# Performance work log

Measured on AMD Instinct MI355X. Metric: run time of the kernel, lower is better.

Reference implementation:

```python
import jax, jax.numpy as jnp
import numpy as np

N_NODES = 100000
N_EDGES = 1600000
N_GRAPHS = 4096
IN_FEATS = 64
HIDDEN = 128


def setup_inputs() -> dict:
    key = jax.random.key(0)
    ks = jax.random.split(key, 16)
    feats_node = jax.random.normal(ks[0], (N_NODES, IN_FEATS), dtype=jnp.float32)
    feats_graph = jax.random.normal(ks[1], (N_GRAPHS, 3), dtype=jnp.float32)
    src = jax.random.randint(ks[2], (N_EDGES,), 0, N_NODES, dtype=jnp.int32)
    dst = jax.random.randint(ks[3], (N_EDGES,), 0, N_NODES, dtype=jnp.int32)
    node2graph = jnp.sort(jax.random.randint(ks[4], (N_NODES,), 0, N_GRAPHS, dtype=jnp.int32))
    # weights stored as [in, out] (torch Linear W.T); init per module: std=0.5 weights, bias ~ N(0.01, 0.001)
    def w(k, shape):
        return jax.random.normal(k, shape, dtype=jnp.float32) * 0.5
    def b(k, shape):
        return 0.01 + 0.001 * jax.random.normal(k, shape, dtype=jnp.float32)
    return {
        'feats_node': feats_node, 'feats_graph': feats_graph,
        'src': src, 'dst': dst, 'node2graph': node2graph,
        'W1': w(ks[5], (IN_FEATS, HIDDEN)), 'b1': b(ks[6], (HIDDEN,)),
        'W2': w(ks[7], (HIDDEN, HIDDEN)), 'b2': b(ks[8], (HIDDEN,)),
        'W3': w(ks[9], (HIDDEN, HIDDEN)), 'b3': b(ks[10], (HIDDEN,)),
        'L1w': w(ks[11], (HIDDEN + 3, 2 * HIDDEN)), 'L1b': b(ks[12], (2 * HIDDEN,)),
        'L2w': w(ks[13], (2 * HIDDEN, HIDDEN)), 'L2b': b(ks[14], (HIDDEN,)),
        'L3w': w(ks[15], (HIDDEN, 1)), 'L3b': b(jax.random.fold_in(key, 99), (1,)),
    }


def _graph_conv(x, W, b, src, dst, norm_out, norm_in):
    # DGL GraphConv(norm='both'): h_i = (sum_{j->i} x_j * d_out(j)^-1/2) * d_in(i)^-1/2 @ W + b
    m = (x * norm_out)[src]                       # [E, F] gather
    agg = jax.ops.segment_sum(m, dst, num_segments=N_NODES)
    return (agg * norm_in) @ W + b


def reference(feats_node, feats_graph, W1, b1, W2, b2, W3, b3, L1w, L1b, L2w, L2b, L3w, L3b, src, dst, node2graph):
    ones = jnp.ones((N_EDGES,), dtype=jnp.float32)
    deg_out = jax.ops.segment_sum(ones, src, num_segments=N_NODES)
    deg_in = jax.ops.segment_sum(ones, dst, num_segments=N_NODES)
    norm_out = jnp.clip(deg_out, 1.0, None)[:, None] ** -0.5  # [N,1]
    norm_in = jnp.clip(deg_in, 1.0, None)[:, None] ** -0.5

    x = jax.nn.selu(_graph_conv(feats_node, W1, b1, src, dst, norm_out, norm_in))
    x = jax.nn.selu(_graph_conv(x, W2, b2, src, dst, norm_out, norm_in))
    y_node = _graph_conv(x, W3, b3, src, dst, norm_out, norm_in)

    y_sum = jax.ops.segment_sum(y_node, node2graph, num_segments=N_GRAPHS)  # readout 'sum'
    y = jnp.concatenate([y_sum, feats_graph], axis=1)  # [G, H+3]
    y = jax.nn.selu(y @ L1w + L1b)
    y = jax.nn.selu(y @ L2w + L2b)
    return (y @ L3w + L3b).reshape(-1)
```

## Files before the change

kernel.cpp:

```cpp
#include <hip/hip_runtime.h>
#include <math.h>

#define SELU_ALPHA 1.6732632423543772f
#define SELU_SCALE 1.0507009873554805f

#define NBLK 512
#define MAXBKT 512

typedef __attribute__((ext_vector_type(8))) short bf16x8;
typedef __attribute__((ext_vector_type(4))) float f32x4;

__device__ __forceinline__ float selu_f(float x) {
    return SELU_SCALE * (x > 0.f ? x : SELU_ALPHA * expm1f(x));
}

__device__ __forceinline__ float bf2f(unsigned short u) {
    return __uint_as_float(((unsigned)u) << 16);
}
__device__ __forceinline__ unsigned short f2bf(float f) {
    unsigned u = __float_as_uint(f);
    unsigned r = (u + 0x7fffu + ((u >> 16) & 1u)) >> 16;
    return (unsigned short)r;
}

#define SCAN_B 1024

__global__ __launch_bounds__(256) void scan_block_sums(const int* __restrict__ in,
                                                       int* __restrict__ bsums, int n) {
    __shared__ int s[256];
    int b = blockIdx.x, t = threadIdx.x;
    int base = b * SCAN_B;
    int sum = 0;
    for (int i = t; i < SCAN_B; i += 256) {
        int idx = base + i;
        sum += (idx < n) ? in[idx] : 0;
    }
    s[t] = sum; __syncthreads();
    for (int off = 128; off > 0; off >>= 1) {
        if (t < off) s[t] += s[t + off];
        __syncthreads();
    }
    if (t == 0) bsums[b] = s[0];
}

__global__ __launch_bounds__(256) void scan_apply2(const int* __restrict__ in,
                                                   const int* __restrict__ bsums,
                                                   int* __restrict__ out, int n, int nb) {
    __shared__ int sb[512];
    __shared__ int s[256];
    __shared__ int blockoff;
    int b = blockIdx.x, t = threadIdx.x;

    int orig0 = (t < nb) ? bsums[t] : 0;
    int orig1 = (t + 256 < nb) ? bsums[t + 256] : 0;
    sb[t] = orig0; sb[t + 256] = orig1;
    __syncthreads();
    for (int off = 1; off < 512; off <<= 1) {
        int v0 = (t >= off) ? sb[t - off] : 0;
        int v1 = (t + 256 >= off) ? sb[t + 256 - off] : 0;
        __syncthreads();
        sb[t] += v0; sb[t + 256] += v1;
        __syncthreads();
    }
    if (t == (b & 255)) {
        bool hi = b >= 256;
        int incl = hi ? sb[t + 256] : sb[t];
        int orig = hi ? orig1 : orig0;
        blockoff = incl - orig;
    }
    __syncthreads();

    int idx0 = b * SCAN_B + t * 4;
    int v[4]; int tsum = 0;
    #pragma unroll
    for (int k = 0; k < 4; ++k) {
        int idx = idx0 + k;
        v[k] = (idx < n) ? in[idx] : 0;
        tsum += v[k];
    }
    s[t] = tsum; __syncthreads();
    for (int off = 1; off < 256; off <<= 1) {
        int x = (t >= off) ? s[t - off] : 0;
        __syncthreads();
        s[t] += x;
        __syncthreads();
    }
    int run = s[t] - tsum + blockoff;
    #pragma unroll
    for (int k = 0; k < 4; ++k) {
        int idx = idx0 + k;
        if (idx < n) out[idx] = run;
        run += v[k];
    }
}

__global__ __launch_bounds__(256) void hist_prep_kernel(
        const int* __restrict__ src, const int* __restrict__ dst,
        int* __restrict__ cntD, int* __restrict__ cntS, int E, int nbkt,
        const float* __restrict__ W1, const float* __restrict__ W2,
        const float* __restrict__ W3, const float* __restrict__ b3,
        const float* __restrict__ L1w, const float* __restrict__ L2w,
        unsigned short* __restrict__ Wt1, unsigned short* __restrict__ Wt2,
        unsigned short* __restrict__ W1c, unsigned short* __restrict__ L2w16) {
    if (blockIdx.x >= NBLK) {
        const int s0 = 128 * 64;
        const int s1 = 128 * 128;
        const int s2 = 128 * 256;
        const int s3 = 3 * 256;
        const int s4 = 256;
        const int s5 = 256 * 128 / 4;
        int i = (blockIdx.x - NBLK) * 256 + threadIdx.x;
        if (i < s0) { int col = i / 64, k = i % 64; Wt1[i] = f2bf(W1[k * 128 + col]); return; }
        i -= s0;
        if (i < s1) { int col = i / 128, k = i % 128; Wt2[i] = f2bf(W2[k * 128 + col]); return; }
        i -= s1;
        if (i < s2) {
            int k = i >> 8, o = i & 255;
            float acc = 0.f;
            #pragma unroll 8
            for (int m = 0; m < 128; ++m)
                acc += W3[k * 128 + m] * L1w[m * 256 + o];
            W1c[k * 256 + o] = f2bf(acc);
            return;
        }
        i -= s2;
        if (i < s3) {
            int r = i >> 8, o = i & 255;
            W1c[(128 + r) * 256 + o] = f2bf(L1w[(128 + r) * 256 + o]);
            return;
        }
        i -= s3;
        if (i < s4) {
            int o = i;
            float acc = 0.f;
            #pragma unroll 8
            for (int m = 0; m < 128; ++m)
                acc += b3[m] * L1w[m * 256 + o];
            W1c[131 * 256 + o] = f2bf(acc);
            return;
        }
        i -= s4;
        if (i < s5) {
            float4 v = reinterpret_cast<const float4*>(L2w)[i];
            unsigned short o[4] = { f2bf(v.x), f2bf(v.y), f2bf(v.z), f2bf(v.w) };
            reinterpret_cast<uint2*>(L2w16)[i] = *reinterpret_cast<uint2*>(o);
        }
        return;
    }
    __shared__ int hD[MAXBKT];
    __shared__ int hS[MAXBKT];
    int bb = blockIdx.x, t = threadIdx.x;
    for (int k = t; k < MAXBKT; k += 256) { hD[k] = 0; hS[k] = 0; }
    __syncthreads();
    int chunk = E / NBLK;
    int beg = bb * chunk, end = beg + chunk;
    for (int i = beg + t; i < end; i += 256) {
        atomicAdd(&hD[((unsigned)dst[i]) >> 8], 1);
        atomicAdd(&hS[((unsigned)src[i]) >> 8], 1);
    }
    __syncthreads();
    for (int k = t; k < nbkt; k += 256) {
        cntD[k * NBLK + bb] = hD[k];
        cntS[k * NBLK + bb] = hS[k];
    }
}

__global__ __launch_bounds__(256) void scatter_kernel(
        const int* __restrict__ src, const int* __restrict__ dst,
        const int* __restrict__ cntD, const int* __restrict__ cntS,
        unsigned* __restrict__ pairs, int* __restrict__ sbufm, int E, int nbkt) {
    __shared__ int cD[MAXBKT];
    __shared__ int cS[MAXBKT];
    int bb = blockIdx.x, t = threadIdx.x;
    for (int k = t; k < nbkt; k += 256) {
        cD[k] = cntD[k * NBLK + bb];
        cS[k] = cntS[k * NBLK + bb];
    }
    __syncthreads();
    int chunk = E / NBLK;
    int beg = bb * chunk, end = beg + chunk;
    for (int i = beg + t; i < end; i += 256) {
        unsigned s = (unsigned)src[i], d = (unsigned)dst[i];
        int pD = atomicAdd(&cD[d >> 8], 1);
        pairs[pD] = s | ((d & 255u) << 24);
        int pS = atomicAdd(&cS[s >> 8], 1);
        sbufm[pS] = (int)s;
    }
}

__global__ __launch_bounds__(256) void bucket_build_kernel(
        const int* __restrict__ sbufm, const unsigned* __restrict__ pairs,
        const int* __restrict__ cntD, const int* __restrict__ cntS,
        const float* __restrict__ feats,
        float* __restrict__ norm_out, unsigned short* __restrict__ feats16,
        int* __restrict__ row_start, int* __restrict__ deg_in,
        int* __restrict__ csr_src, int N, int E, int nbkt) {
    __shared__ int hist[256];
    __shared__ int sc[256];
    __shared__ int cur[256];
    __shared__ float nrm[256];
    int b = blockIdx.x, t = threadIdx.x;
    int node = (b << 8) + t;
    int node0 = b << 8;

    {
        int base = cntS[b * NBLK];
        int end = (b + 1 < nbkt) ? cntS[(b + 1) * NBLK] : 2 * E;
        hist[t] = 0; __syncthreads();
        for (int i = base + t; i < end; i += 256)
            atomicAdd(&hist[sbufm[i] & 255], 1);
        __syncthreads();
        float no = 1.f / sqrtf(fmaxf((float)hist[t], 1.f));
        nrm[t] = no;
        if (node < N) norm_out[node] = no;
        __syncthreads();
    }

    {
        int cnt = min(256, N - node0);
        for (int i = t; i < cnt * 8; i += 256) {
            int nl = i >> 3, c = i & 7;
            float no = nrm[nl];
            const float* fp = feats + (size_t)(node0 + nl) * 64 + c * 8;
            float4 a = *reinterpret_cast<const float4*>(fp);
            float4 bv = *reinterpret_cast<const float4*>(fp + 4);
            unsigned short o[8] = { f2bf(a.x * no), f2bf(a.y * no), f2bf(a.z * no), f2bf(a.w * no),
                                    f2bf(bv.x * no), f2bf(bv.y * no), f2bf(bv.z * no), f2bf(bv.w * no) };
            *reinterpret_cast<float4*>(feats16 + (size_t)(node0 + nl) * 64 + c * 8) =
                *reinterpret_cast<float4*>(o);
        }
        __syncthreads();
    }

    {
        int base = cntD[b * NBLK];
        int end = (b + 1 < nbkt) ? cntD[(b + 1) * NBLK] : E;
        hist[t] = 0; __syncthreads();
        for (int i = base + t; i < end; i += 256)
            atomicAdd(&hist[(pairs[i] >> 24) & 255], 1);
        __syncthreads();
        int v = hist[t];
        sc[t] = v; __syncthreads();
        for (int off = 1; off < 256; off <<= 1) {
            int x = (t >= off) ? sc[t - off] : 0;
            __syncthreads();
            sc[t] += x;
            __syncthreads();
        }
        int ex = sc[t] - v;
        cur[t] = base + ex;
        if (node < N) { row_start[node] = base + ex; deg_in[node] = v; }
        __syncthreads();
        for (int i = base + t; i < end; i += 256) {
            unsigned p = pairs[i];
            int pos = atomicAdd(&cur[(p >> 24) & 255], 1);
            csr_src[pos] = (int)(p & 0xFFFFFFu);
        }
    }
}

template<int TPG, int FIN>
__global__ __launch_bounds__(256) void csr_agg_kernel(
        const unsigned short* __restrict__ x, const int* __restrict__ row_start,
        const int* __restrict__ deg_in, const int* __restrict__ csr_src,
        unsigned short* __restrict__ agg, int N) {
    const int GPB = 256 / TPG;
    int g = threadIdx.x / TPG;
    int j = threadIdx.x % TPG;
    int n = blockIdx.x * GPB + g;
    if (n >= N) return;
    const int lane = threadIdx.x & 63;
    const int gbase = lane & ~(TPG - 1);
    int beg = row_start[n];
    int dg = deg_in[n];
    int end = beg + dg;
    float nin = 1.f / sqrtf(fmaxf((float)dg, 1.f));
    float acc[8] = {0.f, 0.f, 0.f, 0.f, 0.f, 0.f, 0.f, 0.f};
    int myIdx = (beg + j < end) ? csr_src[beg + j] : 0;
    for (int c = beg; c < end; c += TPG) {
        int cnt = end - c;
        int nxtIdx = (c + TPG + j < end) ? csr_src[c + TPG + j] : 0;
        float4 v[TPG];
        #pragma unroll
        for (int t = 0; t < TPG; ++t) {
            if (t < cnt) {
                int s = __shfl(myIdx, gbase + t, 64);
                v[t] = *reinterpret_cast<const float4*>(&x[(size_t)s * FIN + j * 8]);
            }
        }
        #pragma unroll
        for (int t = 0; t < TPG; ++t) {
            if (t < cnt) {
                const unsigned short* u = reinterpret_cast<const unsigned short*>(&v[t]);
                #pragma unroll
                for (int k = 0; k < 8; ++k) acc[k] += bf2f(u[k]);
            }
        }
        myIdx = nxtIdx;
    }
    unsigned short ov[8];
    #pragma unroll
    for (int k = 0; k < 8; ++k) ov[k] = f2bf(acc[k] * nin);
    *reinterpret_cast<float4*>(&agg[(size_t)n * FIN + j * 8]) = *reinterpret_cast<float4*>(ov);
}

template<int FIN, bool SELU, bool SCALE_OUT>
__global__ __launch_bounds__(256, 4) void gemm_mfma_kernel(
        const unsigned short* __restrict__ agg16,
        const unsigned short* __restrict__ Wt,
        const float* __restrict__ b,
        const float* __restrict__ norm_out,
        unsigned short* __restrict__ out,
        int N) {
    const int PAD = 8;
    const int LDW = FIN + PAD;
    const int CH = FIN / 8;
    __shared__ unsigned short sW[128 * LDW];
    const int tid = threadIdx.x;
    const int wave = tid >> 6, lane = tid & 63;
    const int wr = (wave >> 1) * 64;
    const int wc = (wave & 1) * 64;
    const int n0 = blockIdx.x * 128;

    for (int i = tid; i < 128 * CH; i += 256) {
        int col = i / CH, kc = i % CH;
        *reinterpret_cast<float4*>(&sW[col * LDW + kc * 8]) =
            *reinterpret_cast<const float4*>(&Wt[col * FIN + kc * 8]);
    }
    __syncthreads();

    const int l16 = lane & 15;
    const int lk = (lane >> 4) * 8;
    const bf16x8 zero8 = (bf16x8){0,0,0,0,0,0,0,0};
    f32x4 acc[4][4];
    #pragma unroll
    for (int mi = 0; mi < 4; ++mi)
        #pragma unroll
        for (int ci = 0; ci < 4; ++ci)
            acc[mi][ci] = (f32x4){0.f, 0.f, 0.f, 0.f};

    #pragma unroll
    for (int k0 = 0; k0 < FIN; k0 += 32) {
        bf16x8 a[4], w[4];
        #pragma unroll
        for (int mi = 0; mi < 4; ++mi) {
            int n = n0 + wr + mi * 16 + l16;
            a[mi] = (n < N)
                ? *reinterpret_cast<const bf16x8*>(&agg16[(size_t)n * FIN + k0 + lk])
                : zero8;
        }
        #pragma unroll
        for (int ci = 0; ci < 4; ++ci)
            w[ci] = *reinterpret_cast<const bf16x8*>(&sW[(wc + ci * 16 + l16) * LDW + k0 + lk]);
        #pragma unroll
        for (int mi = 0; mi < 4; ++mi)
            #pragma unroll
            for (int ci = 0; ci < 4; ++ci)
                acc[mi][ci] = __builtin_amdgcn_mfma_f32_16x16x32_bf16(
                    a[mi], w[ci], acc[mi][ci], 0, 0, 0);
    }

    const int rbase = (lane >> 4) * 4;
    #pragma unroll
    for (int ci = 0; ci < 4; ++ci) {
        int col = wc + ci * 16 + l16;
        float bias = b[col];
        #pragma unroll
        for (int mi = 0; mi < 4; ++mi) {
            #pragma unroll
            for (int r = 0; r < 4; ++r) {
                int n = n0 + wr + mi * 16 + rbase + r;
                if (n < N) {
                    float v = acc[mi][ci][r] + bias;
                    if (SELU) v = selu_f(v);
                    if (SCALE_OUT) v *= norm_out[n];
                    out[(size_t)n * 128 + col] = f2bf(v);
                }
            }
        }
    }
}

__global__ __launch_bounds__(128) void readout_kernel(
        const unsigned short* __restrict__ y, const int* __restrict__ n2g,
        float* __restrict__ gsum, float* __restrict__ cntf, int N, int G) {
    int g = blockIdx.x;
    int o = threadIdx.x;
    if (g >= G) return;
    int beg, end;
    {
        int lo = 0, hi = N;
        while (lo < hi) { int m = (lo + hi) >> 1; if (n2g[m] < g) lo = m + 1; else hi = m; }
        beg = lo;
        lo = beg; hi = N;
        while (lo < hi) { int m = (lo + hi) >> 1; if (n2g[m] < g + 1) lo = m + 1; else hi = m; }
        end = lo;
    }
    float acc = 0.f;
    for (int n = beg; n < end; ++n)
        acc += bf2f(y[(size_t)n * 128 + o]);
    gsum[(size_t)g * 128 + o] = acc;
    if (o == 0) cntf[g] = (float)(end - beg);
}

__global__ __launch_bounds__(256) void mlp_head_kernel(
        const float* __restrict__ gsum, const float* __restrict__ fg,
        const float* __restrict__ cntf,
        const unsigned short* __restrict__ W1c,
        const float* __restrict__ L1b,
        const unsigned short* __restrict__ L2w16,
        const float* __restrict__ L2b,
        const float* __restrict__ L3w, const float* __restrict__ L3b,
        float* __restrict__ out, int G) {
    __shared__ unsigned short sW[132 * 256];
    __shared__ float sIn[16][132];
    __shared__ float sY1[16][256];
    __shared__ float sL3[128];
    __shared__ float red[16][2];
    int tid = threadIdx.x;
    int g0 = blockIdx.x * 16;

    for (int i = tid; i < 132 * 256 / 2; i += 256)
        reinterpret_cast<unsigned*>(sW)[i] = reinterpret_cast<const unsigned*>(W1c)[i];
    for (int i = tid; i < 16 * 132; i += 256) {
        int g = i / 132, k = i - g * 132;
        float v = 0.f;
        if (g0 + g < G) {
            if (k < 128)       v = gsum[(size_t)(g0 + g) * 128 + k];
            else if (k < 131)  v = fg[(size_t)(g0 + g) * 3 + (k - 128)];
            else               v = cntf[g0 + g];
        }
        sIn[g][k] = v;
    }
    __syncthreads();
    {
        float bias = L1b[tid];
        for (int g = 0; g < 16; ++g) {
            float acc = bias;
            #pragma unroll 4
            for (int k = 0; k < 132; ++k)
                acc += sIn[g][k] * bf2f(sW[k * 256 + tid]);
            sY1[g][tid] = selu_f(acc);
        }
    }
    __syncthreads();

    for (int i = tid; i < 256 * 128 / 2; i += 256)
        reinterpret_cast<unsigned*>(sW)[i] = reinterpret_cast<const unsigned*>(L2w16)[i];
    if (tid < 128) sL3[tid] = L3w[tid];
    __syncthreads();
    {
        int o = tid & 127;
        int half = tid >> 7;
        int lane = tid & 63;
        int wv = tid >> 6;
        float bias = L2b[o];
        float w3 = sL3[o];
        for (int gg = 0; gg < 8; ++gg) {
            int g = half * 8 + gg;
            float acc = bias;
            #pragma unroll 8
            for (int k = 0; k < 256; ++k)
                acc += sY1[g][k] * bf2f(sW[k * 128 + o]);
            float v = selu_f(acc) * w3;
            #pragma unroll
            for (int off = 32; off > 0; off >>= 1)
                v += __shfl_down(v, off, 64);
            if (lane == 0) red[g][wv & 1] = v;
        }
    }
    __syncthreads();
    if (tid < 16) {
        int g = g0 + tid;
        if (g < G) out[g] = red[tid][0] + red[tid][1] + L3b[0];
    }
}

extern "C" void kernel_launch(void* const* d_in, const int* in_sizes, int n_in,
                              void* d_out, int out_size, void* d_ws, size_t ws_size,
                              hipStream_t stream) {
    const float* feats_node  = (const float*)d_in[0];
    const float* feats_graph = (const float*)d_in[1];
    const int*   src         = (const int*)d_in[2];
    const int*   dst         = (const int*)d_in[3];
    const int*   node2graph  = (const int*)d_in[4];
    const float* W1 = (const float*)d_in[5];
    const float* b1 = (const float*)d_in[6];
    const float* W2 = (const float*)d_in[7];
    const float* b2 = (const float*)d_in[8];
    const float* W3 = (const float*)d_in[9];
    const float* b3 = (const float*)d_in[10];
    const float* L1w = (const float*)d_in[11];
    const float* L1b = (const float*)d_in[12];
    const float* L2w = (const float*)d_in[13];
    const float* L2b = (const float*)d_in[14];
    const float* L3w = (const float*)d_in[15];
    const float* L3b = (const float*)d_in[16];

    const int N = in_sizes[0] / 64;
    const int G = in_sizes[1] / 3;
    const int E = in_sizes[2];
    const int NBKT = (N + 255) >> 8;
    const int nmat = NBKT * NBLK;
    const int nscan = 2 * nmat;
    const int NBsc = (nscan + SCAN_B - 1) / SCAN_B;

    int* iws = (int*)d_ws;
    int* deg_in_i  = iws;
    int* row_start = deg_in_i + N;
    int* bsums     = row_start + N;
    int* cntD      = bsums + 512;
    int* cntS      = cntD + nmat;
    int* csr_src   = cntS + nmat;

    float* norm_out = (float*)(csr_src + E);

    unsigned short* feats16 = (unsigned short*)(norm_out + N);
    unsigned short* x16     = feats16 + (size_t)N * 64;
    unsigned short* agg16   = x16 + (size_t)N * 128;
    unsigned short* Wt1     = agg16 + (size_t)N * 128;
    unsigned short* Wt2     = Wt1 + 128 * 64;
    unsigned short* W1c     = Wt2 + 128 * 128;
    unsigned short* L2w16   = W1c + 132 * 256;

    float* gsum = (float*)(L2w16 + 256 * 128);
    float* cntf = gsum + (size_t)G * 128;

    unsigned* pairs = (unsigned*)(((uintptr_t)agg16 + 15) & ~(uintptr_t)15);
    int*      sbuf  = (int*)(pairs + E);
    int*      sbufm = sbuf - E;

    float* out = (float*)d_out;

    {
        const int wtotal = 128 * 64 + 128 * 128 + 128 * 256 + 3 * 256 + 256 + 256 * 128 / 4;
        const int wblocks = (wtotal + 255) / 256;
        hist_prep_kernel<<<NBLK + wblocks, 256, 0, stream>>>(
            src, dst, cntD, cntS, E, NBKT,
            W1, W2, W3, b3, L1w, L2w, Wt1, Wt2, W1c, L2w16);
    }

    scan_block_sums<<<NBsc, 256, 0, stream>>>(cntD, bsums, nscan);
    scan_apply2<<<NBsc, 256, 0, stream>>>(cntD, bsums, cntD, nscan, NBsc);
    scatter_kernel<<<NBLK, 256, 0, stream>>>(src, dst, cntD, cntS, pairs, sbufm, E, NBKT);

    bucket_build_kernel<<<NBKT, 256, 0, stream>>>(
        sbufm, pairs, cntD, cntS, feats_node,
        norm_out, feats16, row_start, deg_in_i, csr_src, N, E, NBKT);

    const int gemm_grid = (N + 127) / 128;

    csr_agg_kernel<8, 64><<<(N + 31) / 32, 256, 0, stream>>>(
        feats16, row_start, deg_in_i, csr_src, agg16, N);
    gemm_mfma_kernel<64, true, true><<<gemm_grid, 256, 0, stream>>>(
        agg16, Wt1, b1, norm_out, x16, N);

    csr_agg_kernel<16, 128><<<(N + 15) / 16, 256, 0, stream>>>(
        x16, row_start, deg_in_i, csr_src, agg16, N);
    gemm_mfma_kernel<128, true, true><<<gemm_grid, 256, 0, stream>>>(
        agg16, Wt2, b2, norm_out, x16, N);

    csr_agg_kernel<16, 128><<<(N + 15) / 16, 256, 0, stream>>>(
        x16, row_start, deg_in_i, csr_src, agg16, N);

    readout_kernel<<<G, 128, 0, stream>>>(agg16, node2graph, gsum, cntf, N, G);

    mlp_head_kernel<<<(G + 15) / 16, 256, 0, stream>>>(
        gsum, feats_graph, cntf, W1c, L1b, L2w16, L2b, L3w, L3b, out, G);
}
```

Before: 382.0 us.

## Fuse graph readout and MLP head into one per-graph kernel

Merges the readout kernel and the batched MLP head into one kernel with one block per graph. Each block sums its node rows with two halves, then runs the L1 and L2 layers reading weights straight from global memory/L2 instead of staging them in LDS. This removes a launch and the gsum/cntf round trip through global memory. In exchange, every graph block re-reads the full weight matrices (about 130 KB) through cache, where before one staged copy served 16 graphs.

```diff
diff --git a/kernel.cpp b/kernel.cpp
--- a/kernel.cpp
+++ b/kernel.cpp
@@ -381,12 +381,24 @@
     }
 }
 
-__global__ __launch_bounds__(128) void readout_kernel(
-        const unsigned short* __restrict__ y, const int* __restrict__ n2g,
-        float* __restrict__ gsum, float* __restrict__ cntf, int N, int G) {
+__global__ __launch_bounds__(256) void head_kernel(
+        const unsigned short* __restrict__ agg16,
+        const int* __restrict__ n2g,
+        const float* __restrict__ fg,
+        const unsigned short* __restrict__ W1c,
+        const float* __restrict__ L1b,
+        const unsigned short* __restrict__ L2w16,
+        const float* __restrict__ L2b,
+        const float* __restrict__ L3w, const float* __restrict__ L3b,
+        float* __restrict__ out, int N, int G) {
+    __shared__ float sIn[132];
+    __shared__ float sY1[256];
+    __shared__ float sPair[256];
+    __shared__ float sRed[2];
     int g = blockIdx.x;
-    int o = threadIdx.x;
     if (g >= G) return;
+    int tid = threadIdx.x;
+
     int beg, end;
     {
         int lo = 0, hi = N;
@@ -396,84 +408,47 @@
         while (lo < hi) { int m = (lo + hi) >> 1; if (n2g[m] < g + 1) lo = m + 1; else hi = m; }
         end = lo;
     }
-    float acc = 0.f;
-    for (int n = beg; n < end; ++n)
-        acc += bf2f(y[(size_t)n * 128 + o]);
-    gsum[(size_t)g * 128 + o] = acc;
-    if (o == 0) cntf[g] = (float)(end - beg);
-}
-
-__global__ __launch_bounds__(256) void mlp_head_kernel(
-        const float* __restrict__ gsum, const float* __restrict__ fg,
-        const float* __restrict__ cntf,
-        const unsigned short* __restrict__ W1c,
-        const float* __restrict__ L1b,
-        const unsigned short* __restrict__ L2w16,
-        const float* __restrict__ L2b,
-        const float* __restrict__ L3w, const float* __restrict__ L3b,
-        float* __restrict__ out, int G) {
-    __shared__ unsigned short sW[132 * 256];
-    __shared__ float sIn[16][132];
-    __shared__ float sY1[16][256];
-    __shared__ float sL3[128];
-    __shared__ float red[16][2];
-    int tid = threadIdx.x;
-    int g0 = blockIdx.x * 16;
-
-    for (int i = tid; i < 132 * 256 / 2; i += 256)
-        reinterpret_cast<unsigned*>(sW)[i] = reinterpret_cast<const unsigned*>(W1c)[i];
-    for (int i = tid; i < 16 * 132; i += 256) {
-        int g = i / 132, k = i - g * 132;
-        float v = 0.f;
-        if (g0 + g < G) {
-            if (k < 128)       v = gsum[(size_t)(g0 + g) * 128 + k];
-            else if (k < 131)  v = fg[(size_t)(g0 + g) * 3 + (k - 128)];
-            else               v = cntf[g0 + g];
-        }
-        sIn[g][k] = v;
-    }
-    __syncthreads();
-    {
-        float bias = L1b[tid];
-        for (int g = 0; g < 16; ++g) {
-            float acc = bias;
-            #pragma unroll 4
-            for (int k = 0; k < 132; ++k)
-                acc += sIn[g][k] * bf2f(sW[k * 256 + tid]);
-            sY1[g][tid] = selu_f(acc);
-        }
-    }
-    __syncthreads();
-
-    for (int i = tid; i < 256 * 128 / 2; i += 256)
-        reinterpret_cast<unsigned*>(sW)[i] = reinterpret_cast<const unsigned*>(L2w16)[i];
-    if (tid < 128) sL3[tid] = L3w[tid];
-    __syncthreads();
-    {
-        int o = tid & 127;
-        int half = tid >> 7;
-        int lane = tid & 63;
-        int wv = tid >> 6;
-        float bias = L2b[o];
-        float w3 = sL3[o];
-        for (int gg = 0; gg < 8; ++gg) {
-            int g = half * 8 + gg;
-            float acc = bias;
-            #pragma unroll 8
-            for (int k = 0; k < 256; ++k)
-                acc += sY1[g][k] * bf2f(sW[k * 128 + o]);
-            float v = selu_f(acc) * w3;
-            #pragma unroll
-            for (int off = 32; off > 0; off >>= 1)
-                v += __shfl_down(v, off, 64);
-            if (lane == 0) red[g][wv & 1] = v;
-        }
-    }
-    __syncthreads();
-    if (tid < 16) {
-        int g = g0 + tid;
-        if (g < G) out[g] = red[tid][0] + red[tid][1] + L3b[0];
-    }
+    {
+        int col = tid & 127, h = tid >> 7;
+        float acc = 0.f;
+        for (int n = beg + h; n < end; n += 2)
+            acc += bf2f(agg16[(size_t)n * 128 + col]);
+        sPair[tid] = acc;
+    }
+    __syncthreads();
+    if (tid < 128) sIn[tid] = sPair[tid] + sPair[tid + 128];
+    else if (tid < 131) sIn[tid] = fg[(size_t)g * 3 + (tid - 128)];
+    else if (tid == 131) sIn[131] = (float)(end - beg);
+    __syncthreads();
+
+    {
+        float acc = L1b[tid];
+        #pragma unroll 4
+        for (int k = 0; k < 132; ++k)
+            acc += sIn[k] * bf2f(W1c[k * 256 + tid]);
+        sY1[tid] = selu_f(acc);
+    }
+    __syncthreads();
+
+    {
+        int o = tid & 127, h = tid >> 7;
+        float acc = 0.f;
+        int k0 = h * 128;
+        #pragma unroll 8
+        for (int k = 0; k < 128; ++k)
+            acc += sY1[k0 + k] * bf2f(L2w16[(k0 + k) * 128 + o]);
+        sPair[tid] = acc;
+    }
+    __syncthreads();
+    if (tid < 128) {
+        float y2 = selu_f(sPair[tid] + sPair[tid + 128] + L2b[tid]) * L3w[tid];
+        #pragma unroll
+        for (int off = 32; off > 0; off >>= 1)
+            y2 += __shfl_down(y2, off, 64);
+        if ((tid & 63) == 0) sRed[tid >> 6] = y2;
+    }
+    __syncthreads();
+    if (tid == 0) out[g] = sRed[0] + sRed[1] + L3b[0];
 }
 
 extern "C" void kernel_launch(void* const* d_in, const int* in_sizes, int n_in,
@@ -523,9 +498,6 @@
     unsigned short* W1c     = Wt2 + 128 * 128;
     unsigned short* L2w16   = W1c + 132 * 256;
 
-    float* gsum = (float*)(L2w16 + 256 * 128);
-    float* cntf = gsum + (size_t)G * 128;
-
     unsigned* pairs = (unsigned*)(((uintptr_t)agg16 + 15) & ~(uintptr_t)15);
     int*      sbuf  = (int*)(pairs + E);
     int*      sbufm = sbuf - E;
@@ -563,8 +535,6 @@
     csr_agg_kernel<16, 128><<<(N + 15) / 16, 256, 0, stream>>>(
         x16, row_start, deg_in_i, csr_src, agg16, N);
 
-    readout_kernel<<<G, 128, 0, stream>>>(agg16, node2graph, gsum, cntf, N, G);
-
-    mlp_head_kernel<<<(G + 15) / 16, 256, 0, stream>>>(
-        gsum, feats_graph, cntf, W1c, L1b, L2w16, L2b, L3w, L3b, out, G);
-}
+    head_kernel<<<G, 256, 0, stream>>>(
+        agg16, node2graph, feats_graph, W1c, L1b, L2w16, L2b, L3w, L3b, out, N, G);
+}
```

Measured after the change: 344.3 us. 1.11x faster.
